# Performance work log

Measured on AMD Instinct MI355X. Metric: run time of the kernel, lower is better.

## Reference

```python
import jax, jax.numpy as jnp
import numpy as np

B, T, D, U = 128, 256, 256, 1024


def setup_inputs() -> dict:
    key = jax.random.key(0)
    ks = jax.random.split(key, 5)
    features = jax.random.normal(ks[0], (B, T, D), dtype=jnp.float32)
    # irregular positive time deltas in (0, 1)
    time_steps = jax.random.uniform(ks[1], (B, T), dtype=jnp.float32)
    scale_x = 1.0 / np.sqrt(D)
    scale_h = 1.0 / np.sqrt(U)
    Wx = jax.random.normal(ks[2], (D, 2 * U), dtype=jnp.float32) * scale_x
    Wh = jax.random.normal(ks[3], (U, 2 * U), dtype=jnp.float32) * scale_h
    b = jnp.zeros((2 * U,), dtype=jnp.float32)
    w_tau = jax.random.uniform(ks[4], (U,), dtype=jnp.float32)
    h0 = jnp.zeros((B, U), dtype=jnp.float32)
    return {"features": features, "time_steps": time_steps, "Wx": Wx,
            "Wh": Wh, "b": b, "w_tau": w_tau, "h0": h0}


def reference(features, time_steps, Wx, Wh, b, w_tau, h0):
    """IrregularRNN with exact closed-form LTC cell, return_sequences=True.

    Per step: f = sigmoid(pre_f), A = tanh(pre_a),
              h' = (h - A) * exp(-dt * (softplus(w_tau) + f)) + A
    """
    tau = jax.nn.softplus(w_tau)  # [U]

    def step(h, xt):
        x_t, dt_t = xt                      # [B,D], [B]
        pre = x_t @ Wx + h @ Wh + b         # [B,2U]
        f = jax.nn.sigmoid(pre[:, :U])
        a = jnp.tanh(pre[:, U:])
        decay = jnp.exp(-dt_t[:, None] * (tau + f))
        h_new = (h - a) * decay + a
        return h_new, h_new

    xs = (jnp.swapaxes(features, 0, 1), jnp.swapaxes(time_steps, 0, 1))
    _, ys = jax.lax.scan(step, h0, xs)      # ys: [T,B,U]
    return jnp.swapaxes(ys, 0, 1)           # [B,T,U]
```

## Files before the change

### kernel.cpp

```cpp
#include <hip/hip_runtime.h>

typedef _Float16 v8h  __attribute__((ext_vector_type(8)));
typedef _Float16 v4h  __attribute__((ext_vector_type(4)));
typedef float    v4f  __attribute__((ext_vector_type(4)));
typedef unsigned int u32x4 __attribute__((ext_vector_type(4)));

#define BATCH   128
#define TSTEPS  256
#define DFEAT   256
#define UDIM    1024
#define NCOL    2048
#define ASTRIDE 1288


__global__ __launch_bounds__(1024)
void ltc_rnn_kernel(const float* __restrict__ features,
                    const float* __restrict__ tsteps,
                    const float* __restrict__ Wx,
                    const float* __restrict__ Wh,
                    const float* __restrict__ bias,
                    const float* __restrict__ wtau,
                    const float* __restrict__ h0,
                    float* __restrict__ out,
                    unsigned* __restrict__ flags,
                    _Float16* __restrict__ hbufs)
{
  __shared__ _Float16 Alds[16 * ASTRIDE];
  __shared__ float    Plds[16 * 64 * 4];
  __shared__ _Float16 Hout[16][32];
  __shared__ float    dtlds[2][16];

  const int tid  = threadIdx.x;
  const int w    = tid >> 6;
  const int lane = tid & 63;
  const int n    = lane & 15;
  const int q    = lane >> 4;
  const int cg   = w & 3;
  const int ks   = w >> 2;
  const int g    = blockIdx.x & 7;
  const int cb   = blockIdx.x >> 3;
  const int u0   = cb * 32;

  const int gcol = (n < 8) ? (u0 + cg * 8 + n) : (UDIM + u0 + cg * 8 + (n - 8));
  v8h bfr[10];
  #pragma unroll
  for (int c = 0; c < 10; ++c) {
    #pragma unroll
    for (int j = 0; j < 8; ++j) {
      const int k = ks * 320 + c * 32 + q * 8 + j;
      const float wv = (k < DFEAT) ? Wx[(size_t)k * NCOL + gcol]
                                   : Wh[(size_t)(k - DFEAT) * NCOL + gcol];
      bfr[c][j] = (_Float16)wv;
    }
  }

  const float bias_own = bias[gcol];
  const int   u_lane   = u0 + cg * 8 + (n & 7);
  const float tau      = logf(1.0f + __expf(wtau[u_lane]));

  float h_reg[4];
  #pragma unroll
  for (int i = 0; i < 4; ++i)
    h_reg[i] = h0[(size_t)(g * 16 + q * 4 + i) * UDIM + u_lane];

  if (tid < 16) dtlds[0][tid] = tsteps[(size_t)(g * 16 + tid) * TSTEPS + 0];
  {
    const int r = tid >> 6, k4 = tid & 63;
    v4f x4 = *(const v4f*)(features + (size_t)(g * 16 + r) * (TSTEPS * DFEAT) + k4 * 4);
    v4h xh = {(_Float16)x4.x, (_Float16)x4.y, (_Float16)x4.z, (_Float16)x4.w};
    *(v4h*)&Alds[r * ASTRIDE + k4 * 4] = xh;
    #pragma unroll
    for (int jj = 0; jj < 4; ++jj) {
      const int c = tid + jj * 1024, hr = c >> 8, hk4 = c & 255;
      v4f h4 = *(const v4f*)(h0 + (size_t)(g * 16 + hr) * UDIM + hk4 * 4);
      v4h hh = {(_Float16)h4.x, (_Float16)h4.y, (_Float16)h4.z, (_Float16)h4.w};
      *(v4h*)&Alds[hr * ASTRIDE + DFEAT + hk4 * 4] = hh;
    }
  }
  __syncthreads();

  for (int t = 0; t < TSTEPS; ++t) {
    const bool more = (t + 1 < TSTEPS);
    _Float16* hdst = hbufs + ((t + 1) & 1) * (BATCH * UDIM);

    {
      v4f acc0 = {0.f, 0.f, 0.f, 0.f};
      v4f acc1 = {0.f, 0.f, 0.f, 0.f};
      const _Float16* abase = &Alds[n * ASTRIDE + ks * 320 + q * 8];
      #pragma unroll
      for (int c = 0; c < 10; c += 2) {
        v8h a0 = *(const v8h*)(abase + c * 32);
        v8h a1 = *(const v8h*)(abase + (c + 1) * 32);
        acc0 = __builtin_amdgcn_mfma_f32_16x16x32_f16(a0, bfr[c],     acc0, 0, 0, 0);
        acc1 = __builtin_amdgcn_mfma_f32_16x16x32_f16(a1, bfr[c + 1], acc1, 0, 0, 0);
      }
      v4f acc = acc0 + acc1;
      *(v4f*)&Plds[(w * 64 + lane) * 4] = acc;
    }
    __syncthreads();

    float outv[4];
    if (w < 4) {
      v4f p = *(v4f*)&Plds[((0 * 4 + w) * 64 + lane) * 4];
      #pragma unroll
      for (int s = 1; s < 4; ++s) {
        v4f ps = *(v4f*)&Plds[((s * 4 + w) * 64 + lane) * 4];
        p.x += ps.x; p.y += ps.y; p.z += ps.z; p.w += ps.w;
      }
      float pf[4], pa[4];
      #pragma unroll
      for (int i = 0; i < 4; ++i) {
        const float v = p[i] + bias_own;
        const float o = __shfl_xor(v, 8);
        pf[i] = v; pa[i] = o;
      }
      if (n < 8) {
        #pragma unroll
        for (int i = 0; i < 4; ++i) {
          const int   row_l = q * 4 + i;
          const float dt    = dtlds[t & 1][row_l];
          const float f     = 1.0f / (1.0f + __expf(-pf[i]));
          const float av    = 2.0f / (1.0f + __expf(-2.0f * pa[i])) - 1.0f;
          const float decay = __expf(-dt * (tau + f));
          const float hn    = (h_reg[i] - av) * decay + av;
          h_reg[i] = hn;
          outv[i]  = hn;
          Hout[row_l][w * 8 + n] = (_Float16)hn;
        }
      }
    }
    __syncthreads();

    if (w == 0 && more) {
      const int row = lane >> 2, c8 = lane & 3;
      v8h hv = *(v8h*)&Hout[row][c8 * 8];
      _Float16* dp = hdst + (size_t)(g * 16 + row) * UDIM + u0 + c8 * 8;
      asm volatile("global_store_dwordx4 %0, %1, off sc0 sc1\n\t"
                   "s_waitcnt vmcnt(0)"
                   :: "v"(dp), "v"(__builtin_bit_cast(u32x4, hv)) : "memory");
      if (lane == 0) {
        unsigned tg = (unsigned)(t + 1);
        asm volatile("global_store_dword %0, %1, off sc0 sc1"
                     :: "v"(&flags[g * 64 + cb]), "v"(tg) : "memory");
      }
    }

    const unsigned* fp = &flags[g * 64 + (lane & 31)];
    unsigned v0 = 0;
    if (more) {
      asm volatile("global_load_dword %0, %1, off sc0 sc1"
                   : "=v"(v0) : "v"(fp) : "memory");
    }

    if (w < 4 && n < 8) {
      #pragma unroll
      for (int i = 0; i < 4; ++i) {
        const int row = g * 16 + q * 4 + i;
        out[(size_t)row * (TSTEPS * UDIM) + (size_t)t * UDIM + u_lane] = outv[i];
      }
    }
    if (more) {
      if (tid < 16) dtlds[(t + 1) & 1][tid] = tsteps[(size_t)(g * 16 + tid) * TSTEPS + t + 1];
      const int r = tid >> 6, k4 = tid & 63;
      v4f x4 = *(const v4f*)(features + (size_t)(g * 16 + r) * (TSTEPS * DFEAT)
                             + (size_t)(t + 1) * DFEAT + k4 * 4);
      v4h xh = {(_Float16)x4.x, (_Float16)x4.y, (_Float16)x4.z, (_Float16)x4.w};
      *(v4h*)&Alds[r * ASTRIDE + k4 * 4] = xh;
    }

    if (more) {
      const unsigned tg = (unsigned)t;
      asm volatile("s_waitcnt vmcnt(0)" : "+v"(v0) :: "memory");
      if (__ballot(v0 <= tg) != 0ull) {
        for (;;) {
          unsigned v;
          asm volatile("global_load_dword %0, %1, off sc0 sc1\n\t"
                       "s_waitcnt vmcnt(0)"
                       : "=v"(v) : "v"(fp) : "memory");
          if (__ballot(v <= tg) == 0ull) break;
        }
      }
      const _Float16* hsrc = hbufs + ((t + 1) & 1) * (BATCH * UDIM);
      const int c0 = tid, c1 = tid + 1024;
      const _Float16* p0 = hsrc + (size_t)(g * 16 + (c0 >> 7)) * UDIM + (c0 & 127) * 8;
      const _Float16* p1 = hsrc + (size_t)(g * 16 + (c1 >> 7)) * UDIM + (c1 & 127) * 8;
      u32x4 r0, r1;
      asm volatile("global_load_dwordx4 %0, %2, off sc0 sc1\n\t"
                   "global_load_dwordx4 %1, %3, off sc0 sc1\n\t"
                   "s_waitcnt vmcnt(0)"
                   : "=v"(r0), "=v"(r1) : "v"(p0), "v"(p1) : "memory");
      *(v8h*)&Alds[(c0 >> 7) * ASTRIDE + DFEAT + (c0 & 127) * 8] = __builtin_bit_cast(v8h, r0);
      *(v8h*)&Alds[(c1 >> 7) * ASTRIDE + DFEAT + (c1 & 127) * 8] = __builtin_bit_cast(v8h, r1);
      __syncthreads();
    }
  }
}

extern "C" void kernel_launch(void* const* d_in, const int* in_sizes, int n_in,
                              void* d_out, int out_size, void* d_ws, size_t ws_size,
                              hipStream_t stream) {
  const float* features = (const float*)d_in[0];
  const float* tsamp    = (const float*)d_in[1];
  const float* Wx       = (const float*)d_in[2];
  const float* Wh       = (const float*)d_in[3];
  const float* bias     = (const float*)d_in[4];
  const float* wtau     = (const float*)d_in[5];
  const float* h0       = (const float*)d_in[6];
  float*     out    = (float*)d_out;
  unsigned*  flags  = (unsigned*)d_ws;
  _Float16*  hbufs  = (_Float16*)((char*)d_ws + 4096);

  hipMemsetAsync(d_ws, 0, 4096, stream);
  hipLaunchKernelGGL(ltc_rnn_kernel, dim3(256), dim3(1024), 0, stream,
                     features, tsamp, Wx, Wh, bias, wtau, h0, out, flags, hbufs);
}
```

Measured before the change: 1.026 ms.

## Replace flag-based grid barrier with self-validating tagged hidden-state packets

Each producer block now packs its new fp16 hidden-state slice into 16-byte packets. Every packet embeds the step tag twice alongside six fp16 values, so consumers can poll the data directly instead of waiting on a separate flag and then loading the data. It also swaps the block-wide barrier after the cell update for an LDS atomic counter, so only the two packing waves wait for the four compute waves. The point is to remove a round-trip and a serialized store-then-flag sequence from the per-step cross-block sync. The cost is a larger zeroed workspace, more complex deposit logic, and a fallback to the old kernel when the workspace is too small.

```diff
diff --git a/kernel.cpp b/kernel.cpp
--- a/kernel.cpp
+++ b/kernel.cpp
@@ -12,6 +12,12 @@
 #define NCOL    2048
 #define ASTRIDE 1288
 
+#define NPKT    86
+#define PKT_DW  4
+#define PROD_DW (NPKT * PKT_DW)
+#define PAR_DW  (8 * 32 * PROD_DW)
+#define PKT_BYTES (2u * 352256u)
+#define TOTPKT  (32 * NPKT)
 
 __global__ __launch_bounds__(1024)
 void ltc_rnn_kernel(const float* __restrict__ features,
@@ -22,13 +28,13 @@
                     const float* __restrict__ wtau,
                     const float* __restrict__ h0,
                     float* __restrict__ out,
-                    unsigned* __restrict__ flags,
-                    _Float16* __restrict__ hbufs)
+                    unsigned* __restrict__ pkt)
 {
   __shared__ _Float16 Alds[16 * ASTRIDE];
   __shared__ float    Plds[16 * 64 * 4];
-  __shared__ _Float16 Hout[16][32];
+  __shared__ _Float16 HoutL[528];
   __shared__ float    dtlds[2][16];
+  __shared__ unsigned hsc;
 
   const int tid  = threadIdx.x;
   const int w    = tid >> 6;
@@ -41,6 +47,8 @@
   const int cb   = blockIdx.x >> 3;
   const int u0   = cb * 32;
 
+  if (tid == 0) hsc = 0u;
+
   const int gcol = (n < 8) ? (u0 + cg * 8 + n) : (UDIM + u0 + cg * 8 + (n - 8));
   v8h bfr[10];
   #pragma unroll
@@ -62,6 +70,27 @@
   #pragma unroll
   for (int i = 0; i < 4; ++i)
     h_reg[i] = h0[(size_t)(g * 16 + q * 4 + i) * UDIM + u_lane];
+
+  int cPA[3], cPB[3], cJS[3], cNV[3];
+  const unsigned* cSRC[3];
+  bool cFAST[3];
+  #pragma unroll
+  for (int k = 0; k < 3; ++k) {
+    const int pi  = tid + k * 1024;
+    const bool act = pi < TOTPKT;
+    const int pic = act ? pi : tid;
+    const int cbp = pic / NPKT;
+    const int p   = pic - cbp * NPKT;
+    cNV[k]  = act ? ((p == 85) ? 2 : 6) : 0;
+    const int idx0 = p * 6, r0 = idx0 >> 5, c0 = idx0 & 31;
+    cJS[k]  = 32 - c0;
+    cPA[k]  = r0 * ASTRIDE + DFEAT + cbp * 32 + c0;
+    cPB[k]  = (r0 + 1) * ASTRIDE + DFEAT + cbp * 32;
+    cFAST[k] = act && (cNV[k] == 6) && (c0 <= 26);
+    cSRC[k] = pkt + (size_t)(g * 32 + cbp) * PROD_DW + (size_t)p * PKT_DW;
+  }
+  const int pp = (w - 4) * 64 + lane;
+  unsigned* pDST = pkt + (size_t)(g * 32 + cb) * PROD_DW + (size_t)(pp < NPKT ? pp : 0) * PKT_DW;
 
   if (tid < 16) dtlds[0][tid] = tsteps[(size_t)(g * 16 + tid) * TSTEPS + 0];
   {
@@ -81,7 +110,8 @@
 
   for (int t = 0; t < TSTEPS; ++t) {
     const bool more = (t + 1 < TSTEPS);
-    _Float16* hdst = hbufs + ((t + 1) & 1) * (BATCH * UDIM);
+    const unsigned tg = (unsigned)(t + 1);
+    const size_t paroff = ((t + 1) & 1) ? (size_t)PAR_DW : 0;
 
     {
       v4f acc0 = {0.f, 0.f, 0.f, 0.f};
@@ -125,12 +155,202 @@
           const float hn    = (h_reg[i] - av) * decay + av;
           h_reg[i] = hn;
           outv[i]  = hn;
+          HoutL[row_l * 32 + w * 8 + n] = (_Float16)hn;
+        }
+      }
+      if (lane == 0)
+        __hip_atomic_fetch_add(&hsc, 1u, __ATOMIC_RELEASE, __HIP_MEMORY_SCOPE_WORKGROUP);
+    }
+
+    if (w < 4 && n < 8) {
+      #pragma unroll
+      for (int i = 0; i < 4; ++i) {
+        const int row = g * 16 + q * 4 + i;
+        out[(size_t)row * (TSTEPS * UDIM) + (size_t)t * UDIM + u_lane] = outv[i];
+      }
+    }
+
+    if (more) {
+      if (tid < 16) dtlds[(t + 1) & 1][tid] = tsteps[(size_t)(g * 16 + tid) * TSTEPS + t + 1];
+      const int r = tid >> 6, k4 = tid & 63;
+      v4f x4 = *(const v4f*)(features + (size_t)(g * 16 + r) * (TSTEPS * DFEAT)
+                             + (size_t)(t + 1) * DFEAT + k4 * 4);
+      v4h xh = {(_Float16)x4.x, (_Float16)x4.y, (_Float16)x4.z, (_Float16)x4.w};
+      *(v4h*)&Alds[r * ASTRIDE + k4 * 4] = xh;
+    }
+
+    if (more && (w == 4 || w == 5)) {
+      const unsigned target = 4u * (unsigned)(t + 1);
+      while (__hip_atomic_load(&hsc, __ATOMIC_ACQUIRE, __HIP_MEMORY_SCOPE_WORKGROUP) < target) {}
+      if (pp < NPKT) {
+        const unsigned* Hw = (const unsigned*)HoutL;
+        const unsigned s0 = Hw[3 * pp], s1 = Hw[3 * pp + 1], s2 = Hw[3 * pp + 2];
+        u32x4 pk;
+        pk.x = tg | (s0 << 16);
+        pk.y = (s0 >> 16) | (s1 << 16);
+        pk.z = tg | (s1 & 0xffff0000u);
+        pk.w = s2;
+        unsigned* dst = pDST + paroff;
+        asm volatile("global_store_dwordx4 %0, %1, off sc0 sc1"
+                     :: "v"(dst), "v"(pk) : "memory");
+      }
+    }
+
+    if (more) {
+      const unsigned* s0p = cSRC[0] + paroff;
+      const unsigned* s1p = cSRC[1] + paroff;
+      const unsigned* s2p = cSRC[2] + paroff;
+      bool d0 = (cNV[0] == 0), d1 = (cNV[1] == 0), d2 = (cNV[2] == 0);
+      u32x4 ra, rb, rc;
+
+#define EXTRACT_H(R, J) ((J) == 0 ? ((R).x >> 16) : (J) == 1 ? ((R).y & 0xffffu) : \
+                         (J) == 2 ? ((R).y >> 16) : (J) == 3 ? ((R).z >> 16) : \
+                         (J) == 4 ? ((R).w & 0xffffu) : ((R).w >> 16))
+#define DEPOSIT(K, R)                                                              \
+      do {                                                                         \
+        if (cFAST[K]) {                                                            \
+          unsigned short* b = (unsigned short*)Alds + cPA[K];                      \
+          *(unsigned*)(b)     = ((R).x >> 16) | ((R).y << 16);                     \
+          *(unsigned*)(b + 2) = ((R).y >> 16) | ((R).z & 0xffff0000u);             \
+          *(unsigned*)(b + 4) = (R).w;                                             \
+        } else {                                                                   \
+          _Pragma("unroll")                                                        \
+          for (int j = 0; j < 6; ++j) {                                            \
+            if (j < cNV[K]) {                                                      \
+              const unsigned hv = EXTRACT_H(R, j);                                 \
+              const int a = (j < cJS[K]) ? (cPA[K] + j) : (cPB[K] + (j - cJS[K])); \
+              ((unsigned short*)Alds)[a] = (unsigned short)hv;                     \
+            }                                                                      \
+          }                                                                        \
+        }                                                                          \
+      } while (0)
+
+      for (;;) {
+        asm volatile("global_load_dwordx4 %0, %3, off sc0 sc1\n\t"
+                     "global_load_dwordx4 %1, %4, off sc0 sc1\n\t"
+                     "global_load_dwordx4 %2, %5, off sc0 sc1\n\t"
+                     "s_waitcnt vmcnt(0)"
+                     : "=&v"(ra), "=&v"(rb), "=&v"(rc)
+                     : "v"(s0p), "v"(s1p), "v"(s2p) : "memory");
+        if (!d0 && ((ra.x & 0xffffu) == tg) && ((ra.z & 0xffffu) == tg)) { DEPOSIT(0, ra); d0 = true; }
+        if (!d1 && ((rb.x & 0xffffu) == tg) && ((rb.z & 0xffffu) == tg)) { DEPOSIT(1, rb); d1 = true; }
+        if (!d2 && ((rc.x & 0xffffu) == tg) && ((rc.z & 0xffffu) == tg)) { DEPOSIT(2, rc); d2 = true; }
+        if (d0 && d1 && d2) break;
+      }
+#undef DEPOSIT
+#undef EXTRACT_H
+      __syncthreads();
+    }
+  }
+}
+
+__global__ __launch_bounds__(1024)
+void ltc_rnn_fallback(const float* __restrict__ features, const float* __restrict__ tsteps,
+                      const float* __restrict__ Wx, const float* __restrict__ Wh,
+                      const float* __restrict__ bias, const float* __restrict__ wtau,
+                      const float* __restrict__ h0, float* __restrict__ out,
+                      unsigned* __restrict__ flags, _Float16* __restrict__ hbufs)
+{
+  __shared__ _Float16 Alds[16 * ASTRIDE];
+  __shared__ float    Plds[16 * 64 * 4];
+  __shared__ _Float16 Hout[16][32];
+  __shared__ float    dtlds[2][16];
+
+  const int tid  = threadIdx.x;
+  const int w    = tid >> 6;
+  const int lane = tid & 63;
+  const int n    = lane & 15;
+  const int q    = lane >> 4;
+  const int cg   = w & 3;
+  const int ks   = w >> 2;
+  const int g    = blockIdx.x & 7;
+  const int cb   = blockIdx.x >> 3;
+  const int u0   = cb * 32;
+
+  const int gcol = (n < 8) ? (u0 + cg * 8 + n) : (UDIM + u0 + cg * 8 + (n - 8));
+  v8h bfr[10];
+  #pragma unroll
+  for (int c = 0; c < 10; ++c) {
+    #pragma unroll
+    for (int j = 0; j < 8; ++j) {
+      const int k = ks * 320 + c * 32 + q * 8 + j;
+      const float wv = (k < DFEAT) ? Wx[(size_t)k * NCOL + gcol]
+                                   : Wh[(size_t)(k - DFEAT) * NCOL + gcol];
+      bfr[c][j] = (_Float16)wv;
+    }
+  }
+  const float bias_own = bias[gcol];
+  const int   u_lane   = u0 + cg * 8 + (n & 7);
+  const float tau      = logf(1.0f + __expf(wtau[u_lane]));
+  float h_reg[4];
+  #pragma unroll
+  for (int i = 0; i < 4; ++i)
+    h_reg[i] = h0[(size_t)(g * 16 + q * 4 + i) * UDIM + u_lane];
+
+  if (tid < 16) dtlds[0][tid] = tsteps[(size_t)(g * 16 + tid) * TSTEPS + 0];
+  {
+    const int r = tid >> 6, k4 = tid & 63;
+    v4f x4 = *(const v4f*)(features + (size_t)(g * 16 + r) * (TSTEPS * DFEAT) + k4 * 4);
+    v4h xh = {(_Float16)x4.x, (_Float16)x4.y, (_Float16)x4.z, (_Float16)x4.w};
+    *(v4h*)&Alds[r * ASTRIDE + k4 * 4] = xh;
+    #pragma unroll
+    for (int jj = 0; jj < 4; ++jj) {
+      const int c = tid + jj * 1024, hr = c >> 8, hk4 = c & 255;
+      v4f h4 = *(const v4f*)(h0 + (size_t)(g * 16 + hr) * UDIM + hk4 * 4);
+      v4h hh = {(_Float16)h4.x, (_Float16)h4.y, (_Float16)h4.z, (_Float16)h4.w};
+      *(v4h*)&Alds[hr * ASTRIDE + DFEAT + hk4 * 4] = hh;
+    }
+  }
+  __syncthreads();
+
+  for (int t = 0; t < TSTEPS; ++t) {
+    const bool more = (t + 1 < TSTEPS);
+    _Float16* hdst = hbufs + ((t + 1) & 1) * (BATCH * UDIM);
+    {
+      v4f acc0 = {0.f, 0.f, 0.f, 0.f};
+      v4f acc1 = {0.f, 0.f, 0.f, 0.f};
+      const _Float16* abase = &Alds[n * ASTRIDE + ks * 320 + q * 8];
+      #pragma unroll
+      for (int c = 0; c < 10; c += 2) {
+        v8h a0 = *(const v8h*)(abase + c * 32);
+        v8h a1 = *(const v8h*)(abase + (c + 1) * 32);
+        acc0 = __builtin_amdgcn_mfma_f32_16x16x32_f16(a0, bfr[c],     acc0, 0, 0, 0);
+        acc1 = __builtin_amdgcn_mfma_f32_16x16x32_f16(a1, bfr[c + 1], acc1, 0, 0, 0);
+      }
+      v4f acc = acc0 + acc1;
+      *(v4f*)&Plds[(w * 64 + lane) * 4] = acc;
+    }
+    __syncthreads();
+    float outv[4];
+    if (w < 4) {
+      v4f p = *(v4f*)&Plds[((0 * 4 + w) * 64 + lane) * 4];
+      #pragma unroll
+      for (int s = 1; s < 4; ++s) {
+        v4f ps = *(v4f*)&Plds[((s * 4 + w) * 64 + lane) * 4];
+        p.x += ps.x; p.y += ps.y; p.z += ps.z; p.w += ps.w;
+      }
+      float pf[4], pa[4];
+      #pragma unroll
+      for (int i = 0; i < 4; ++i) {
+        const float v = p[i] + bias_own;
+        const float o = __shfl_xor(v, 8);
+        pf[i] = v; pa[i] = o;
+      }
+      if (n < 8) {
+        #pragma unroll
+        for (int i = 0; i < 4; ++i) {
+          const int   row_l = q * 4 + i;
+          const float dt    = dtlds[t & 1][row_l];
+          const float f     = 1.0f / (1.0f + __expf(-pf[i]));
+          const float av    = 2.0f / (1.0f + __expf(-2.0f * pa[i])) - 1.0f;
+          const float decay = __expf(-dt * (tau + f));
+          const float hn    = (h_reg[i] - av) * decay + av;
+          h_reg[i] = hn; outv[i] = hn;
           Hout[row_l][w * 8 + n] = (_Float16)hn;
         }
       }
     }
     __syncthreads();
-
     if (w == 0 && more) {
       const int row = lane >> 2, c8 = lane & 3;
       v8h hv = *(v8h*)&Hout[row][c8 * 8];
@@ -139,19 +359,17 @@
                    "s_waitcnt vmcnt(0)"
                    :: "v"(dp), "v"(__builtin_bit_cast(u32x4, hv)) : "memory");
       if (lane == 0) {
-        unsigned tg = (unsigned)(t + 1);
+        unsigned tgv = (unsigned)(t + 1);
         asm volatile("global_store_dword %0, %1, off sc0 sc1"
-                     :: "v"(&flags[g * 64 + cb]), "v"(tg) : "memory");
-      }
-    }
-
+                     :: "v"(&flags[g * 64 + cb]), "v"(tgv) : "memory");
+      }
+    }
     const unsigned* fp = &flags[g * 64 + (lane & 31)];
     unsigned v0 = 0;
     if (more) {
       asm volatile("global_load_dword %0, %1, off sc0 sc1"
                    : "=v"(v0) : "v"(fp) : "memory");
     }
-
     if (w < 4 && n < 8) {
       #pragma unroll
       for (int i = 0; i < 4; ++i) {
@@ -167,17 +385,16 @@
       v4h xh = {(_Float16)x4.x, (_Float16)x4.y, (_Float16)x4.z, (_Float16)x4.w};
       *(v4h*)&Alds[r * ASTRIDE + k4 * 4] = xh;
     }
-
     if (more) {
-      const unsigned tg = (unsigned)t;
+      const unsigned tgc = (unsigned)t;
       asm volatile("s_waitcnt vmcnt(0)" : "+v"(v0) :: "memory");
-      if (__ballot(v0 <= tg) != 0ull) {
+      if (__ballot(v0 <= tgc) != 0ull) {
         for (;;) {
           unsigned v;
           asm volatile("global_load_dword %0, %1, off sc0 sc1\n\t"
                        "s_waitcnt vmcnt(0)"
                        : "=v"(v) : "v"(fp) : "memory");
-          if (__ballot(v <= tg) == 0ull) break;
+          if (__ballot(v <= tgc) == 0ull) break;
         }
       }
       const _Float16* hsrc = hbufs + ((t + 1) & 1) * (BATCH * UDIM);
@@ -206,11 +423,19 @@
   const float* bias     = (const float*)d_in[4];
   const float* wtau     = (const float*)d_in[5];
   const float* h0       = (const float*)d_in[6];
-  float*     out    = (float*)d_out;
-  unsigned*  flags  = (unsigned*)d_ws;
-  _Float16*  hbufs  = (_Float16*)((char*)d_ws + 4096);
-
-  hipMemsetAsync(d_ws, 0, 4096, stream);
-  hipLaunchKernelGGL(ltc_rnn_kernel, dim3(256), dim3(1024), 0, stream,
-                     features, tsamp, Wx, Wh, bias, wtau, h0, out, flags, hbufs);
+  float* out = (float*)d_out;
+
+  const size_t need = 4096 + (size_t)PKT_BYTES;
+  if (ws_size >= need) {
+    unsigned* pkt = (unsigned*)((char*)d_ws + 4096);
+    hipMemsetAsync(d_ws, 0, need, stream);
+    hipLaunchKernelGGL(ltc_rnn_kernel, dim3(256), dim3(1024), 0, stream,
+                       features, tsamp, Wx, Wh, bias, wtau, h0, out, pkt);
+  } else {
+    unsigned*  flags = (unsigned*)d_ws;
+    _Float16*  hbufs = (_Float16*)((char*)d_ws + 4096);
+    hipMemsetAsync(d_ws, 0, 4096, stream);
+    hipLaunchKernelGGL(ltc_rnn_fallback, dim3(256), dim3(1024), 0, stream,
+                       features, tsamp, Wx, Wh, bias, wtau, h0, out, flags, hbufs);
+  }
 }
```

New measurement: 1.371 ms. +33.7%, slower.

## Specialize waves and replace block barrier with LDS flags for h exchange

Applied to the files above, without the earlier changes.

Removes the __syncthreads between the cell update and the cross-block hidden-state publish. A dedicated wave now waits on an LDS counter before storing its h slice and flag, and another dedicated wave pipelines the global flag polling with two loads in flight, then signals readiness through an LDS flag. The remaining waves prefetch the next step's features and dt at the same time. The aim is to shorten the serial critical path each timestep, at the cost of intra-block spin-waiting and more complex memory-ordering correctness.

```diff
diff --git a/kernel.cpp b/kernel.cpp
--- a/kernel.cpp
+++ b/kernel.cpp
@@ -29,6 +29,8 @@
   __shared__ float    Plds[16 * 64 * 4];
   __shared__ _Float16 Hout[16][32];
   __shared__ float    dtlds[2][16];
+  __shared__ unsigned hsc;
+  __shared__ unsigned hrdy;
 
   const int tid  = threadIdx.x;
   const int w    = tid >> 6;
@@ -40,6 +42,8 @@
   const int g    = blockIdx.x & 7;
   const int cb   = blockIdx.x >> 3;
   const int u0   = cb * 32;
+
+  if (tid == 0) { hsc = 0u; hrdy = 0u; }
 
   const int gcol = (n < 8) ? (u0 + cg * 8 + n) : (UDIM + u0 + cg * 8 + (n - 8));
   v8h bfr[10];
@@ -99,7 +103,6 @@
     }
     __syncthreads();
 
-    float outv[4];
     if (w < 4) {
       v4f p = *(v4f*)&Plds[((0 * 4 + w) * 64 + lane) * 4];
       #pragma unroll
@@ -114,6 +117,7 @@
         const float o = __shfl_xor(v, 8);
         pf[i] = v; pa[i] = o;
       }
+      float outv[4];
       if (n < 8) {
         #pragma unroll
         for (int i = 0; i < 4; ++i) {
@@ -128,58 +132,81 @@
           Hout[row_l][w * 8 + n] = (_Float16)hn;
         }
       }
-    }
-    __syncthreads();
-
-    if (w == 0 && more) {
-      const int row = lane >> 2, c8 = lane & 3;
-      v8h hv = *(v8h*)&Hout[row][c8 * 8];
-      _Float16* dp = hdst + (size_t)(g * 16 + row) * UDIM + u0 + c8 * 8;
-      asm volatile("global_store_dwordx4 %0, %1, off sc0 sc1\n\t"
-                   "s_waitcnt vmcnt(0)"
-                   :: "v"(dp), "v"(__builtin_bit_cast(u32x4, hv)) : "memory");
-      if (lane == 0) {
-        unsigned tg = (unsigned)(t + 1);
-        asm volatile("global_store_dword %0, %1, off sc0 sc1"
-                     :: "v"(&flags[g * 64 + cb]), "v"(tg) : "memory");
-      }
-    }
-
-    const unsigned* fp = &flags[g * 64 + (lane & 31)];
-    unsigned v0 = 0;
+      if (lane == 0)
+        __hip_atomic_fetch_add(&hsc, 1u, __ATOMIC_RELEASE, __HIP_MEMORY_SCOPE_WORKGROUP);
+      if (n < 8) {
+        #pragma unroll
+        for (int i = 0; i < 4; ++i) {
+          const int row = g * 16 + q * 4 + i;
+          out[(size_t)row * (TSTEPS * UDIM) + (size_t)t * UDIM + u_lane] = outv[i];
+        }
+      }
+      if (more) {
+        v4f x4 = *(const v4f*)(features + (size_t)(g * 16 + w) * (TSTEPS * DFEAT)
+                               + (size_t)(t + 1) * DFEAT + lane * 4);
+        v4h xh = {(_Float16)x4.x, (_Float16)x4.y, (_Float16)x4.z, (_Float16)x4.w};
+        *(v4h*)&Alds[w * ASTRIDE + lane * 4] = xh;
+      }
+    } else if (w == 4) {
+      if (more) {
+        const unsigned target = 4u * (unsigned)(t + 1);
+        while (__hip_atomic_load(&hsc, __ATOMIC_ACQUIRE, __HIP_MEMORY_SCOPE_WORKGROUP) < target) {}
+        const int row = lane >> 2, c8 = lane & 3;
+        v8h hv = *(v8h*)&Hout[row][c8 * 8];
+        _Float16* dp = hdst + (size_t)(g * 16 + row) * UDIM + u0 + c8 * 8;
+        asm volatile("global_store_dwordx4 %0, %1, off sc0 sc1\n\t"
+                     "s_waitcnt vmcnt(0)"
+                     :: "v"(dp), "v"(__builtin_bit_cast(u32x4, hv)) : "memory");
+        if (lane == 0) {
+          unsigned tgv = (unsigned)(t + 1);
+          asm volatile("global_store_dword %0, %1, off sc0 sc1"
+                       :: "v"(&flags[g * 64 + cb]), "v"(tgv) : "memory");
+        }
+        #pragma unroll
+        for (int rr = 0; rr < 2; ++rr) {
+          const int row2 = rr ? 15 : 4;
+          v4f x4 = *(const v4f*)(features + (size_t)(g * 16 + row2) * (TSTEPS * DFEAT)
+                                 + (size_t)(t + 1) * DFEAT + lane * 4);
+          v4h xh = {(_Float16)x4.x, (_Float16)x4.y, (_Float16)x4.z, (_Float16)x4.w};
+          *(v4h*)&Alds[row2 * ASTRIDE + lane * 4] = xh;
+        }
+      }
+    } else if (w == 15) {
+      if (more) {
+        const unsigned* fp = &flags[g * 64 + (lane & 31)];
+        const unsigned  tg = (unsigned)t;
+        unsigned va, vb;
+        asm volatile("global_load_dword %0, %1, off sc0 sc1"
+                     : "=v"(va) : "v"(fp) : "memory");
+        for (;;) {
+          asm volatile("global_load_dword %0, %1, off sc0 sc1"
+                       : "=v"(vb) : "v"(fp) : "memory");
+          asm volatile("s_waitcnt vmcnt(1)" : "+v"(va) :: "memory");
+          if (__ballot(va <= tg) == 0ull) break;
+          asm volatile("global_load_dword %0, %1, off sc0 sc1"
+                       : "=v"(va) : "v"(fp) : "memory");
+          asm volatile("s_waitcnt vmcnt(1)" : "+v"(vb) :: "memory");
+          if (__ballot(vb <= tg) == 0ull) break;
+        }
+        asm volatile("s_waitcnt vmcnt(0)" ::: "memory");
+        if (lane == 0)
+          __hip_atomic_store(&hrdy, (unsigned)(t + 1), __ATOMIC_RELEASE,
+                             __HIP_MEMORY_SCOPE_WORKGROUP);
+      }
+    } else {
+      if (more) {
+        if (w == 14 && lane < 16)
+          dtlds[(t + 1) & 1][lane] = tsteps[(size_t)(g * 16 + lane) * TSTEPS + t + 1];
+        v4f x4 = *(const v4f*)(features + (size_t)(g * 16 + w) * (TSTEPS * DFEAT)
+                               + (size_t)(t + 1) * DFEAT + lane * 4);
+        v4h xh = {(_Float16)x4.x, (_Float16)x4.y, (_Float16)x4.z, (_Float16)x4.w};
+        *(v4h*)&Alds[w * ASTRIDE + lane * 4] = xh;
+      }
+    }
+
     if (more) {
-      asm volatile("global_load_dword %0, %1, off sc0 sc1"
-                   : "=v"(v0) : "v"(fp) : "memory");
-    }
-
-    if (w < 4 && n < 8) {
-      #pragma unroll
-      for (int i = 0; i < 4; ++i) {
-        const int row = g * 16 + q * 4 + i;
-        out[(size_t)row * (TSTEPS * UDIM) + (size_t)t * UDIM + u_lane] = outv[i];
-      }
-    }
-    if (more) {
-      if (tid < 16) dtlds[(t + 1) & 1][tid] = tsteps[(size_t)(g * 16 + tid) * TSTEPS + t + 1];
-      const int r = tid >> 6, k4 = tid & 63;
-      v4f x4 = *(const v4f*)(features + (size_t)(g * 16 + r) * (TSTEPS * DFEAT)
-                             + (size_t)(t + 1) * DFEAT + k4 * 4);
-      v4h xh = {(_Float16)x4.x, (_Float16)x4.y, (_Float16)x4.z, (_Float16)x4.w};
-      *(v4h*)&Alds[r * ASTRIDE + k4 * 4] = xh;
-    }
-
-    if (more) {
-      const unsigned tg = (unsigned)t;
-      asm volatile("s_waitcnt vmcnt(0)" : "+v"(v0) :: "memory");
-      if (__ballot(v0 <= tg) != 0ull) {
-        for (;;) {
-          unsigned v;
-          asm volatile("global_load_dword %0, %1, off sc0 sc1\n\t"
-                       "s_waitcnt vmcnt(0)"
-                       : "=v"(v) : "v"(fp) : "memory");
-          if (__ballot(v <= tg) == 0ull) break;
-        }
-      }
+      while (__hip_atomic_load(&hrdy, __ATOMIC_ACQUIRE, __HIP_MEMORY_SCOPE_WORKGROUP)
+             < (unsigned)(t + 1)) {}
       const _Float16* hsrc = hbufs + ((t + 1) & 1) * (BATCH * UDIM);
       const int c0 = tid, c1 = tid + 1024;
       const _Float16* p0 = hsrc + (size_t)(g * 16 + (c0 >> 7)) * UDIM + (c0 & 127) * 8;
```

After: 1.242 ms. 21.0% more time.

## Reassign MFMA work so each wave computes two column tiles over shorter K

Applied to the files above, without the earlier changes.

Each of the 16 waves now covers two 8+8 column tiles over a 160-wide K slice, instead of one tile over a 320-wide slice. Each A fragment loaded from LDS is reused for two MFMAs, which halves the per-step LDS reads of the A matrix. The cost is an 8-way instead of 4-way partial-sum reduction, with twice as many Plds writes and reads done by the first four waves. Hout is also padded to 40 columns, likely to cut LDS bank conflicts.

```diff
diff --git a/kernel.cpp b/kernel.cpp
--- a/kernel.cpp
+++ b/kernel.cpp
@@ -26,8 +26,8 @@
                     _Float16* __restrict__ hbufs)
 {
   __shared__ _Float16 Alds[16 * ASTRIDE];
-  __shared__ float    Plds[16 * 64 * 4];
-  __shared__ _Float16 Hout[16][32];
+  __shared__ float    Plds[8 * 4 * 64 * 4];
+  __shared__ _Float16 Hout[16][40];
   __shared__ float    dtlds[2][16];
 
   const int tid  = threadIdx.x;
@@ -35,27 +35,33 @@
   const int lane = tid & 63;
   const int n    = lane & 15;
   const int q    = lane >> 4;
-  const int cg   = w & 3;
-  const int ks   = w >> 2;
+  const int cg   = w & 1;
+  const int ks   = w >> 1;
+  const int we   = w & 3;
   const int g    = blockIdx.x & 7;
   const int cb   = blockIdx.x >> 3;
   const int u0   = cb * 32;
 
-  const int gcol = (n < 8) ? (u0 + cg * 8 + n) : (UDIM + u0 + cg * 8 + (n - 8));
-  v8h bfr[10];
+  v8h bfr[2][5];
   #pragma unroll
-  for (int c = 0; c < 10; ++c) {
+  for (int tt = 0; tt < 2; ++tt) {
+    const int tile = cg * 2 + tt;
+    const int gcolw = (n < 8) ? (u0 + tile * 8 + n) : (UDIM + u0 + tile * 8 + (n - 8));
     #pragma unroll
-    for (int j = 0; j < 8; ++j) {
-      const int k = ks * 320 + c * 32 + q * 8 + j;
-      const float wv = (k < DFEAT) ? Wx[(size_t)k * NCOL + gcol]
-                                   : Wh[(size_t)(k - DFEAT) * NCOL + gcol];
-      bfr[c][j] = (_Float16)wv;
+    for (int c = 0; c < 5; ++c) {
+      #pragma unroll
+      for (int j = 0; j < 8; ++j) {
+        const int k = ks * 160 + c * 32 + q * 8 + j;
+        const float wv = (k < DFEAT) ? Wx[(size_t)k * NCOL + gcolw]
+                                     : Wh[(size_t)(k - DFEAT) * NCOL + gcolw];
+        bfr[tt][c][j] = (_Float16)wv;
+      }
     }
   }
 
-  const float bias_own = bias[gcol];
-  const int   u_lane   = u0 + cg * 8 + (n & 7);
+  const int   gcolE   = (n < 8) ? (u0 + we * 8 + n) : (UDIM + u0 + we * 8 + (n - 8));
+  const float bias_own = bias[gcolE];
+  const int   u_lane   = u0 + we * 8 + (n & 7);
   const float tau      = logf(1.0f + __expf(wtau[u_lane]));
 
   float h_reg[4];
@@ -86,16 +92,15 @@
     {
       v4f acc0 = {0.f, 0.f, 0.f, 0.f};
       v4f acc1 = {0.f, 0.f, 0.f, 0.f};
-      const _Float16* abase = &Alds[n * ASTRIDE + ks * 320 + q * 8];
-      #pragma unroll
-      for (int c = 0; c < 10; c += 2) {
-        v8h a0 = *(const v8h*)(abase + c * 32);
-        v8h a1 = *(const v8h*)(abase + (c + 1) * 32);
-        acc0 = __builtin_amdgcn_mfma_f32_16x16x32_f16(a0, bfr[c],     acc0, 0, 0, 0);
-        acc1 = __builtin_amdgcn_mfma_f32_16x16x32_f16(a1, bfr[c + 1], acc1, 0, 0, 0);
-      }
-      v4f acc = acc0 + acc1;
-      *(v4f*)&Plds[(w * 64 + lane) * 4] = acc;
+      const _Float16* abase = &Alds[n * ASTRIDE + ks * 160 + q * 8];
+      #pragma unroll
+      for (int c = 0; c < 5; ++c) {
+        v8h a = *(const v8h*)(abase + c * 32);
+        acc0 = __builtin_amdgcn_mfma_f32_16x16x32_f16(a, bfr[0][c], acc0, 0, 0, 0);
+        acc1 = __builtin_amdgcn_mfma_f32_16x16x32_f16(a, bfr[1][c], acc1, 0, 0, 0);
+      }
+      *(v4f*)&Plds[((ks * 4 + cg * 2 + 0) * 64 + lane) * 4] = acc0;
+      *(v4f*)&Plds[((ks * 4 + cg * 2 + 1) * 64 + lane) * 4] = acc1;
     }
     __syncthreads();
 
@@ -103,7 +108,7 @@
     if (w < 4) {
       v4f p = *(v4f*)&Plds[((0 * 4 + w) * 64 + lane) * 4];
       #pragma unroll
-      for (int s = 1; s < 4; ++s) {
+      for (int s = 1; s < 8; ++s) {
         v4f ps = *(v4f*)&Plds[((s * 4 + w) * 64 + lane) * 4];
         p.x += ps.x; p.y += ps.y; p.z += ps.z; p.w += ps.w;
       }
```

New measurement: 998.4 us. -2.7%, faster.
